# Performance work log

Hardware: AMD Instinct MI355X
Metric: run time of the kernel (lower is better)

Reference implementation:

```python
import jax, jax.numpy as jnp
import numpy as np
from jax.scipy.linalg import solve_triangular

N, D, E = 100000, 128, 1600000
LAMDA, ALPHA = 0.5, 0.1


def setup_inputs() -> dict:
    key = jax.random.key(0)
    k1, k2, k3, k4, k5, k6 = jax.random.split(key, 6)
    x = jax.random.normal(k1, (N, D), dtype=jnp.float32)
    h0 = jax.random.normal(k2, (N, D), dtype=jnp.float32)
    # glorot_init range for the weight
    init_range = np.sqrt(6.0 / (D + D)).astype(np.float32)
    weight = jax.random.uniform(k3, (D, D), dtype=jnp.float32, minval=-init_range, maxval=init_range)
    adj_vals = jax.random.uniform(k4, (E,), dtype=jnp.float32)  # normalized adjacency values (positive)
    adj_rows = jax.random.randint(k5, (E,), 0, N, dtype=jnp.int32)
    adj_cols = jax.random.randint(k6, (E,), 0, N, dtype=jnp.int32)
    return {"x": x, "h0": h0, "weight": weight, "adj_vals": adj_vals,
            "adj_rows": adj_rows, "adj_cols": adj_cols, "l": 4}


def _ortho_norm(weight):
    d = weight.shape[1]
    wtw = weight.T @ weight + 1e-4 * jnp.eye(d, dtype=weight.dtype)
    L = jnp.linalg.cholesky(wtw)
    # weight @ inv(L).T == (solve(L, weight.T)).T
    return solve_triangular(L, weight.T, lower=True).T


def reference(x, h0, weight, adj_vals, adj_rows, adj_cols, l):
    theta = float(np.log(LAMDA / l + 1.0))
    w_ortho = _ortho_norm(weight)
    # sparse adjacency SpMM: hi[r] = sum_e adj_vals[e] * x[adj_cols[e]] for adj_rows[e]==r
    hi = jax.ops.segment_sum(adj_vals[:, None] * x[adj_cols], adj_rows, num_segments=x.shape[0])
    support = (1.0 - ALPHA) * hi + ALPHA * h0  # variant=False -> r == support
    out = theta * (support @ w_ortho) + (1.0 - theta) * support
    return jnp.tanh(out)  # residual=False
```

## Files before the change

kernel.cpp:

```cpp
#include <hip/hip_runtime.h>
#include <math.h>

#define D 128
#define NB 16
#define RPB 64
#define NBUK_MAX 1024
#define RPBUK 128
#define EPB 16384
#define ALPHA 0.1f
#define LAMDA 0.5f

__global__ __launch_bounds__(256) void wtw_kernel(const float* __restrict__ W,
                                                  float* __restrict__ A) {
    int idx = blockIdx.x * blockDim.x + threadIdx.x;
    int i = idx >> 7, j = idx & (D - 1);
    float acc = (i == j) ? 1e-4f : 0.0f;
#pragma unroll 4
    for (int k = 0; k < D; ++k) acc = fmaf(W[k * D + i], W[k * D + j], acc);
    A[idx] = acc;
}

__global__ __launch_bounds__(256) void chol_factor_kernel(const float* __restrict__ A_in,
                                                          float* __restrict__ Lg) {
    __shared__ float S[D][D];
    __shared__ float dinvS[NB];
    const int tid = threadIdx.x;
    const int tx = tid & 15;
    const int ty = tid >> 4;

    for (int i = tid; i < D * D; i += 256) ((float*)S)[i] = A_in[i];
    __syncthreads();

    for (int s = 0; s < D / NB; ++s) {
        const int b = s * NB;

        for (int k = 0; k < NB; ++k) {
            float dk  = S[b + k][b + k];
            float a_i = S[b + k][b + tx];
            float a_j = S[b + k][b + ty];
            float lkk  = sqrtf(dk);
            float inv  = 1.0f / lkk;
            float invd = inv * inv;
            __syncthreads();
            if (ty == 0) {
                if (tx == k)       { S[b + k][b + k] = lkk; dinvS[k] = inv; }
                else if (tx > k)     S[b + k][b + tx] = a_i * inv;
            }
            if (ty > k && tx >= ty)
                S[b + ty][b + tx] -= a_i * (a_j * invd);
            __syncthreads();
        }

        const int m = D - b - NB;

        if (m > 0 && tid < m) {
            const int r = b + NB + tid;
            float y[NB];
#pragma unroll
            for (int k = 0; k < NB; ++k) y[k] = S[b + k][r];
#pragma unroll
            for (int k = 0; k < NB; ++k) {
                float acc = y[k];
#pragma unroll
                for (int q = 0; q < NB; ++q)
                    if (q < k) acc -= S[b + q][b + k] * y[q];
                y[k] = acc * dinvS[k];
            }
#pragma unroll
            for (int k = 0; k < NB; ++k) S[b + k][r] = y[k];
        }
        __syncthreads();

        const int nt = m >> 4;
        for (int tc = 0; tc < nt; ++tc) {
            for (int tr = tc; tr < nt; ++tr) {
                const int c = b + NB + tc * 16 + ty;
                const int r = b + NB + tr * 16 + tx;
                if (r >= c) {
                    float acc = S[c][r];
#pragma unroll
                    for (int k = 0; k < NB; ++k)
                        acc -= S[b + k][r] * S[b + k][c];
                    S[c][r] = acc;
                }
            }
        }
        __syncthreads();
    }

    for (int i = tid; i < D * D; i += 256) Lg[i] = ((float*)S)[i];
}

__global__ __launch_bounds__(64) void solve_m_kernel(const float* __restrict__ Lg,
                                                     const float* __restrict__ W,
                                                     const int* __restrict__ lp,
                                                     float* __restrict__ Mg) {
    __shared__ float Lr[D][D + 1];
    const int lane = threadIdx.x;
    const int c = blockIdx.x;

    for (int j = 0; j < D; ++j) {
        Lr[lane][j]      = Lg[j * D + lane];
        Lr[lane + 64][j] = Lg[j * D + lane + 64];
    }
    __syncthreads();

    const float w_lo = W[c * D + lane];
    const float w_hi = W[c * D + 64 + lane];
    const float dinv_lo = 1.0f / Lr[lane][lane];
    const float dinv_hi = 1.0f / Lr[lane + 64][lane + 64];
    float y_lo = 0.0f, y_hi = 0.0f;

    for (int i = 0; i < D; ++i) {
        float l0 = Lr[i][lane];
        float l1 = Lr[i][lane + 64];
        float p = 0.0f;
        p += (lane < i)      ? l0 * y_lo : 0.0f;
        p += (lane + 64 < i) ? l1 * y_hi : 0.0f;
#pragma unroll
        for (int off = 32; off >= 1; off >>= 1) p += __shfl_xor(p, off);
        if (i < 64) {
            if (lane == i)      y_lo = (w_lo - p) * dinv_lo;
        } else {
            if (lane == i - 64) y_hi = (w_hi - p) * dinv_hi;
        }
    }

    const float th = logf(LAMDA / (float)(*lp) + 1.0f);
    float m_lo = th * y_lo + ((c == lane)      ? (1.0f - th) : 0.0f);
    float m_hi = th * y_hi + ((c == lane + 64) ? (1.0f - th) : 0.0f);
    Mg[c * D + lane]      = m_lo;
    Mg[c * D + 64 + lane] = m_hi;
}

__global__ __launch_bounds__(256) void cvt_bf16_kernel(const float* __restrict__ x,
                                                       unsigned short* __restrict__ xb,
                                                       int nd) {
    const int base = (blockIdx.x * 256 + threadIdx.x) * 8;
    if (base + 7 < nd) {
        float4 a = *reinterpret_cast<const float4*>(x + base);
        float4 b = *reinterpret_cast<const float4*>(x + base + 4);
        unsigned r[8];
        const float* f = &a.x;
#pragma unroll
        for (int i = 0; i < 4; ++i) {
            unsigned u = __float_as_uint(f[i]);
            r[i] = (u + 0x7FFFu + ((u >> 16) & 1u)) >> 16;
        }
        const float* g = &b.x;
#pragma unroll
        for (int i = 0; i < 4; ++i) {
            unsigned u = __float_as_uint(g[i]);
            r[4 + i] = (u + 0x7FFFu + ((u >> 16) & 1u)) >> 16;
        }
        uint4 o;
        o.x = r[0] | (r[1] << 16);
        o.y = r[2] | (r[3] << 16);
        o.z = r[4] | (r[5] << 16);
        o.w = r[6] | (r[7] << 16);
        *reinterpret_cast<uint4*>(xb + base) = o;
    } else {
        for (int i = 0; i < 8 && base + i < nd; ++i) {
            unsigned u = __float_as_uint(x[base + i]);
            xb[base + i] = (unsigned short)((u + 0x7FFFu + ((u >> 16) & 1u)) >> 16);
        }
    }
}

__global__ __launch_bounds__(256) void count_bucket_kernel(const int* __restrict__ rows,
                                                           int* __restrict__ bcnt,
                                                           int E, int nbuk) {
    __shared__ int lcnt[NBUK_MAX];
    const int tid = threadIdx.x;
    const int e0 = blockIdx.x * EPB;
    const int e1 = min(e0 + EPB, E);
    for (int i = tid; i < nbuk; i += 256) lcnt[i] = 0;
    __syncthreads();
    for (int e = e0 + tid * 4; e < e1; e += 1024) {
        if (e + 3 < e1) {
            int4 r = *reinterpret_cast<const int4*>(rows + e);
            atomicAdd(&lcnt[r.x >> 7], 1);
            atomicAdd(&lcnt[r.y >> 7], 1);
            atomicAdd(&lcnt[r.z >> 7], 1);
            atomicAdd(&lcnt[r.w >> 7], 1);
        } else {
            int lim = min(e + 4, e1);
            for (int k = e; k < lim; ++k) atomicAdd(&lcnt[rows[k] >> 7], 1);
        }
    }
    __syncthreads();
    for (int i = tid; i < nbuk; i += 256) {
        int c = lcnt[i];
        if (c) atomicAdd(&bcnt[i], c);
    }
}

__global__ __launch_bounds__(1024) void scan_bucket_kernel(const int* __restrict__ bcnt,
                                                           int* __restrict__ bbase,
                                                           int* __restrict__ gcur,
                                                           int nbuk) {
    __shared__ int ps[1024];
    const int tid = threadIdx.x;
    int v = (tid < nbuk) ? bcnt[tid] : 0;
    ps[tid] = v;
    __syncthreads();
    for (int off = 1; off < 1024; off <<= 1) {
        int t = (tid >= off) ? ps[tid - off] : 0;
        __syncthreads();
        ps[tid] += t;
        __syncthreads();
    }
    if (tid < nbuk) {
        int excl = ps[tid] - v;
        bbase[tid] = excl;
        gcur[tid]  = excl;
    }
}

__global__ __launch_bounds__(256) void partition_kernel(const int* __restrict__ rows,
                                                        const int* __restrict__ cols,
                                                        const float* __restrict__ vals,
                                                        int* __restrict__ gcur,
                                                        uint2* __restrict__ buk,
                                                        int E, int nbuk) {
    __shared__ int lcnt[NBUK_MAX];
    __shared__ int lbase[NBUK_MAX];
    __shared__ int loff[NBUK_MAX];
    const int tid = threadIdx.x;
    const int e0 = blockIdx.x * EPB;
    const int e1 = min(e0 + EPB, E);
    for (int i = tid; i < nbuk; i += 256) { lcnt[i] = 0; loff[i] = 0; }
    __syncthreads();
    for (int e = e0 + tid * 4; e < e1; e += 1024) {
        if (e + 3 < e1) {
            int4 r = *reinterpret_cast<const int4*>(rows + e);
            atomicAdd(&lcnt[r.x >> 7], 1);
            atomicAdd(&lcnt[r.y >> 7], 1);
            atomicAdd(&lcnt[r.z >> 7], 1);
            atomicAdd(&lcnt[r.w >> 7], 1);
        } else {
            int lim = min(e + 4, e1);
            for (int k = e; k < lim; ++k) atomicAdd(&lcnt[rows[k] >> 7], 1);
        }
    }
    __syncthreads();
    for (int i = tid; i < nbuk; i += 256) {
        int c = lcnt[i];
        if (c) lbase[i] = atomicAdd(&gcur[i], c);
    }
    __syncthreads();
    for (int e = e0 + tid * 4; e < e1; e += 1024) {
        if (e + 3 < e1) {
            int4 r = *reinterpret_cast<const int4*>(rows + e);
            int4 c = *reinterpret_cast<const int4*>(cols + e);
            float4 v = *reinterpret_cast<const float4*>(vals + e);
            {
                int b = r.x >> 7; int li = atomicAdd(&loff[b], 1);
                buk[lbase[b] + li] = make_uint2((unsigned)c.x | ((unsigned)(r.x & 127) << 20), __float_as_uint(v.x));
            }
            {
                int b = r.y >> 7; int li = atomicAdd(&loff[b], 1);
                buk[lbase[b] + li] = make_uint2((unsigned)c.y | ((unsigned)(r.y & 127) << 20), __float_as_uint(v.y));
            }
            {
                int b = r.z >> 7; int li = atomicAdd(&loff[b], 1);
                buk[lbase[b] + li] = make_uint2((unsigned)c.z | ((unsigned)(r.z & 127) << 20), __float_as_uint(v.z));
            }
            {
                int b = r.w >> 7; int li = atomicAdd(&loff[b], 1);
                buk[lbase[b] + li] = make_uint2((unsigned)c.w | ((unsigned)(r.w & 127) << 20), __float_as_uint(v.w));
            }
        } else {
            int lim = min(e + 4, e1);
            for (int k = e; k < lim; ++k) {
                int rr = rows[k];
                int b = rr >> 7; int li = atomicAdd(&loff[b], 1);
                buk[lbase[b] + li] = make_uint2((unsigned)cols[k] | ((unsigned)(rr & 127) << 20), __float_as_uint(vals[k]));
            }
        }
    }
}

__global__ __launch_bounds__(256) void bucket_to_csr_kernel(const uint2* __restrict__ buk,
                                                            const int* __restrict__ bbase,
                                                            const int* __restrict__ bend,
                                                            uint2* __restrict__ csr,
                                                            int* __restrict__ rp, int n) {
    __shared__ int lcnt[RPBUK];
    __shared__ int lofs[RPBUK];
    const int tid = threadIdx.x;
    const int b = blockIdx.x;
    const int start = bbase[b], end = bend[b];

    if (tid < RPBUK) lcnt[tid] = 0;
    __syncthreads();
    for (int j = start + tid; j < end; j += 256)
        atomicAdd(&lcnt[buk[j].x >> 20], 1);
    __syncthreads();
    if (tid < RPBUK) lofs[tid] = lcnt[tid];
    __syncthreads();
    for (int off = 1; off < RPBUK; off <<= 1) {
        int v = (tid < RPBUK && tid >= off) ? lofs[tid - off] : 0;
        __syncthreads();
        if (tid < RPBUK) lofs[tid] += v;
        __syncthreads();
    }
    if (tid < RPBUK) {
        int r = b * RPBUK + tid;
        if (r < n) rp[r] = start + lofs[tid];
        lofs[tid] -= lcnt[tid];
    }
    __syncthreads();
    for (int j = start + tid; j < end; j += 256) {
        uint2 e = buk[j];
        int rl = e.x >> 20;
        int pos = atomicAdd(&lofs[rl], 1);
        csr[start + pos] = make_uint2(e.x & 0xFFFFFu, e.y);
    }
}

__global__ __launch_bounds__(256, 4) void fused_spmm_gemm_kernel(
        const unsigned short* __restrict__ xb,
        const float* __restrict__ h0,
        const uint2* __restrict__ csr,
        const int* __restrict__ rp,
        const float* __restrict__ Mg,
        float* __restrict__ out, int n) {
    __shared__ float Ss[RPB][D + 1];
    const int tid = threadIdx.x;
    const int r0  = blockIdx.x * RPB;
    const int q   = tid & 15;
    const int rw  = tid >> 4;

#pragma unroll
    for (int sub = 0; sub < 4; ++sub) {
        const int sr = sub * 16 + rw;
        const int r  = r0 + sr;
        float acc[8] = {};
        if (r < n) {
            const int start = (r == 0) ? 0 : rp[r - 1];
            const int end   = rp[r];
            int j = start;
            for (; j + 1 < end; j += 2) {
                uint2 p0 = csr[j];
                uint2 p1 = csr[j + 1];
                float v0 = __uint_as_float(p0.y);
                float v1 = __uint_as_float(p1.y);
                uint4 a = *reinterpret_cast<const uint4*>(xb + (size_t)p0.x * D + q * 8);
                uint4 b = *reinterpret_cast<const uint4*>(xb + (size_t)p1.x * D + q * 8);
                const unsigned* aw = &a.x;
                const unsigned* bw = &b.x;
#pragma unroll
                for (int t = 0; t < 4; ++t) {
                    float alo = __uint_as_float(aw[t] << 16);
                    float ahi = __uint_as_float(aw[t] & 0xffff0000u);
                    acc[2 * t]     = fmaf(v0, alo, acc[2 * t]);
                    acc[2 * t + 1] = fmaf(v0, ahi, acc[2 * t + 1]);
                    float blo = __uint_as_float(bw[t] << 16);
                    float bhi = __uint_as_float(bw[t] & 0xffff0000u);
                    acc[2 * t]     = fmaf(v1, blo, acc[2 * t]);
                    acc[2 * t + 1] = fmaf(v1, bhi, acc[2 * t + 1]);
                }
            }
            if (j < end) {
                uint2 p0 = csr[j];
                float v0 = __uint_as_float(p0.y);
                uint4 a = *reinterpret_cast<const uint4*>(xb + (size_t)p0.x * D + q * 8);
                const unsigned* aw = &a.x;
#pragma unroll
                for (int t = 0; t < 4; ++t) {
                    float alo = __uint_as_float(aw[t] << 16);
                    float ahi = __uint_as_float(aw[t] & 0xffff0000u);
                    acc[2 * t]     = fmaf(v0, alo, acc[2 * t]);
                    acc[2 * t + 1] = fmaf(v0, ahi, acc[2 * t + 1]);
                }
            }
            const float4 hb0 = *reinterpret_cast<const float4*>(h0 + (size_t)r * D + q * 8);
            const float4 hb1 = *reinterpret_cast<const float4*>(h0 + (size_t)r * D + q * 8 + 4);
            acc[0] = 0.9f * acc[0] + 0.1f * hb0.x;
            acc[1] = 0.9f * acc[1] + 0.1f * hb0.y;
            acc[2] = 0.9f * acc[2] + 0.1f * hb0.z;
            acc[3] = 0.9f * acc[3] + 0.1f * hb0.w;
            acc[4] = 0.9f * acc[4] + 0.1f * hb1.x;
            acc[5] = 0.9f * acc[5] + 0.1f * hb1.y;
            acc[6] = 0.9f * acc[6] + 0.1f * hb1.z;
            acc[7] = 0.9f * acc[7] + 0.1f * hb1.w;
        }
#pragma unroll
        for (int i = 0; i < 8; ++i) Ss[sr][q * 8 + i] = acc[i];
    }
    __syncthreads();

    const int tc = tid & 15;
    const int tr = tid >> 4;
    float acc2[4][8] = {};
#pragma unroll 8
    for (int k = 0; k < D; ++k) {
        float4 b0 = *reinterpret_cast<const float4*>(Mg + k * D + tc * 4);
        float4 b1 = *reinterpret_cast<const float4*>(Mg + k * D + 64 + tc * 4);
#pragma unroll
        for (int m = 0; m < 4; ++m) {
            float a = Ss[4 * tr + m][k];
            acc2[m][0] = fmaf(a, b0.x, acc2[m][0]);
            acc2[m][1] = fmaf(a, b0.y, acc2[m][1]);
            acc2[m][2] = fmaf(a, b0.z, acc2[m][2]);
            acc2[m][3] = fmaf(a, b0.w, acc2[m][3]);
            acc2[m][4] = fmaf(a, b1.x, acc2[m][4]);
            acc2[m][5] = fmaf(a, b1.y, acc2[m][5]);
            acc2[m][6] = fmaf(a, b1.z, acc2[m][6]);
            acc2[m][7] = fmaf(a, b1.w, acc2[m][7]);
        }
    }

#pragma unroll
    for (int m = 0; m < 4; ++m) {
        int r = r0 + 4 * tr + m;
        if (r >= n) continue;
        float4 o0, o1;
        o0.x = tanhf(acc2[m][0]); o0.y = tanhf(acc2[m][1]);
        o0.z = tanhf(acc2[m][2]); o0.w = tanhf(acc2[m][3]);
        o1.x = tanhf(acc2[m][4]); o1.y = tanhf(acc2[m][5]);
        o1.z = tanhf(acc2[m][6]); o1.w = tanhf(acc2[m][7]);
        *reinterpret_cast<float4*>(out + (size_t)r * D + tc * 4)      = o0;
        *reinterpret_cast<float4*>(out + (size_t)r * D + 64 + tc * 4) = o1;
    }
}

__global__ __launch_bounds__(256) void spmm_atomic_kernel(const float* __restrict__ x,
                                                          const float* __restrict__ vals,
                                                          const int* __restrict__ rows,
                                                          const int* __restrict__ cols,
                                                          float* __restrict__ hi, int E) {
    int tid = blockIdx.x * blockDim.x + threadIdx.x;
    int e = tid >> 5;
    if (e >= E) return;
    int q = tid & 31;
    float v = vals[e];
    int c = cols[e];
    int r = rows[e];
    const float4 xv = *reinterpret_cast<const float4*>(x + (size_t)c * D + q * 4);
    float* h = hi + (size_t)r * D + q * 4;
    unsafeAtomicAdd(h + 0, v * xv.x);
    unsafeAtomicAdd(h + 1, v * xv.y);
    unsafeAtomicAdd(h + 2, v * xv.z);
    unsafeAtomicAdd(h + 3, v * xv.w);
}

__global__ __launch_bounds__(256) void blend_kernel(const float* __restrict__ hi,
                                                    const float* __restrict__ h0,
                                                    float* __restrict__ S, int nd4) {
    int i = blockIdx.x * blockDim.x + threadIdx.x;
    if (i >= nd4) return;
    float4 a = reinterpret_cast<const float4*>(hi)[i];
    float4 b = reinterpret_cast<const float4*>(h0)[i];
    float4 s;
    s.x = 0.9f * a.x + 0.1f * b.x;
    s.y = 0.9f * a.y + 0.1f * b.y;
    s.z = 0.9f * a.z + 0.1f * b.z;
    s.w = 0.9f * a.w + 0.1f * b.w;
    reinterpret_cast<float4*>(S)[i] = s;
}

__global__ __launch_bounds__(256) void gemm_tanh_kernel(const float* __restrict__ S,
                                                        const float* __restrict__ Mg,
                                                        float* __restrict__ out, int n) {
    __shared__ float Ss[RPB][D + 1];
    const int tid = threadIdx.x;
    const int r0  = blockIdx.x * RPB;

    for (int i = tid; i < RPB * D / 4; i += 256) {
        int rr = (i * 4) / D, cc = (i * 4) & (D - 1);
        int r = r0 + rr;
        float4 a = (r < n) ? *reinterpret_cast<const float4*>(S + (size_t)r * D + cc)
                           : make_float4(0.f, 0.f, 0.f, 0.f);
        Ss[rr][cc + 0] = a.x;
        Ss[rr][cc + 1] = a.y;
        Ss[rr][cc + 2] = a.z;
        Ss[rr][cc + 3] = a.w;
    }
    __syncthreads();

    const int tc = tid & 15;
    const int tr = tid >> 4;
    float acc[4][8] = {};
#pragma unroll 8
    for (int k = 0; k < D; ++k) {
        float4 b0 = *reinterpret_cast<const float4*>(Mg + k * D + tc * 4);
        float4 b1 = *reinterpret_cast<const float4*>(Mg + k * D + 64 + tc * 4);
#pragma unroll
        for (int m = 0; m < 4; ++m) {
            float a = Ss[4 * tr + m][k];
            acc[m][0] = fmaf(a, b0.x, acc[m][0]);
            acc[m][1] = fmaf(a, b0.y, acc[m][1]);
            acc[m][2] = fmaf(a, b0.z, acc[m][2]);
            acc[m][3] = fmaf(a, b0.w, acc[m][3]);
            acc[m][4] = fmaf(a, b1.x, acc[m][4]);
            acc[m][5] = fmaf(a, b1.y, acc[m][5]);
            acc[m][6] = fmaf(a, b1.z, acc[m][6]);
            acc[m][7] = fmaf(a, b1.w, acc[m][7]);
        }
    }

#pragma unroll
    for (int m = 0; m < 4; ++m) {
        int r = r0 + 4 * tr + m;
        if (r >= n) continue;
        float4 o0, o1;
        o0.x = tanhf(acc[m][0]); o0.y = tanhf(acc[m][1]);
        o0.z = tanhf(acc[m][2]); o0.w = tanhf(acc[m][3]);
        o1.x = tanhf(acc[m][4]); o1.y = tanhf(acc[m][5]);
        o1.z = tanhf(acc[m][6]); o1.w = tanhf(acc[m][7]);
        *reinterpret_cast<float4*>(out + (size_t)r * D + tc * 4)      = o0;
        *reinterpret_cast<float4*>(out + (size_t)r * D + 64 + tc * 4) = o1;
    }
}

extern "C" void kernel_launch(void* const* d_in, const int* in_sizes, int n_in,
                              void* d_out, int out_size, void* d_ws, size_t ws_size,
                              hipStream_t stream) {
    const float* x  = (const float*)d_in[0];
    const float* h0 = (const float*)d_in[1];
    const float* W  = (const float*)d_in[2];
    const float* av = (const float*)d_in[3];
    const int*   ar = (const int*)d_in[4];
    const int*   ac = (const int*)d_in[5];
    const int*   lp = (const int*)d_in[6];
    float* out = (float*)d_out;

    const int nd = in_sizes[0];
    const int n  = nd / D;
    const int E  = in_sizes[3];
    const int nbuk  = (n + RPBUK - 1) / RPBUK;
    const int nblkE = (E + EPB - 1) / EPB;
    const int grid64 = (n + RPB - 1) / RPB;

    char* wsb = (char*)d_ws;
    float* A  = (float*)wsb;
    float* Lg = A + D * D;
    float* Mg = Lg + D * D;
    size_t off = 3 * (size_t)D * D * sizeof(float);

    int* bcnt  = (int*)(wsb + off); off += NBUK_MAX * sizeof(int);
    int* bbase = (int*)(wsb + off); off += NBUK_MAX * sizeof(int);
    int* gcur  = (int*)(wsb + off); off += NBUK_MAX * sizeof(int);
    off = (off + 15) & ~(size_t)15;
    int* rp = (int*)(wsb + off); off += (size_t)n * sizeof(int);
    off = (off + 15) & ~(size_t)15;
    uint2* csr = (uint2*)(wsb + off); off += (size_t)E * sizeof(uint2);
    off = (off + 15) & ~(size_t)15;
    uint2* buk = (uint2*)(wsb + off); off += (size_t)E * sizeof(uint2);
    off = (off + 15) & ~(size_t)15;
    unsigned short* xb = (unsigned short*)(wsb + off);
    off += (size_t)nd * sizeof(unsigned short);
    off = (off + 15) & ~(size_t)15;
    const size_t need_core = off;

    if (ws_size >= need_core && nbuk <= NBUK_MAX && n < (1 << 20)) {
        hipMemsetAsync(bcnt, 0, NBUK_MAX * sizeof(int), stream);
        count_bucket_kernel<<<nblkE, 256, 0, stream>>>(ar, bcnt, E, nbuk);
        cvt_bf16_kernel<<<(nd / 8 + 255) / 256, 256, 0, stream>>>(x, xb, nd);
        wtw_kernel<<<D * D / 256, 256, 0, stream>>>(W, A);
        scan_bucket_kernel<<<1, 1024, 0, stream>>>(bcnt, bbase, gcur, nbuk);
        partition_kernel<<<nblkE, 256, 0, stream>>>(ar, ac, av, gcur, buk, E, nbuk);
        bucket_to_csr_kernel<<<nbuk, 256, 0, stream>>>(buk, bbase, gcur, csr, rp, n);
        chol_factor_kernel<<<1, 256, 0, stream>>>(A, Lg);
        solve_m_kernel<<<D, 64, 0, stream>>>(Lg, W, lp, Mg);
        fused_spmm_gemm_kernel<<<grid64, 256, 0, stream>>>(xb, h0, csr, rp, Mg, out, n);
    } else {
        float* hi = out;
        hipMemsetAsync(hi, 0, (size_t)nd * sizeof(float), stream);
        wtw_kernel<<<D * D / 256, 256, 0, stream>>>(W, A);
        spmm_atomic_kernel<<<(int)(((size_t)E * 32 + 255) / 256), 256, 0, stream>>>(x, av, ar, ac, hi, E);
        chol_factor_kernel<<<1, 256, 0, stream>>>(A, Lg);
        solve_m_kernel<<<D, 64, 0, stream>>>(Lg, W, lp, Mg);
        blend_kernel<<<(nd / 4 + 255) / 256, 256, 0, stream>>>(hi, h0, hi, nd / 4);
        gemm_tanh_kernel<<<grid64, 256, 0, stream>>>(hi, Mg, out, n);
    }
}
```

Before: 323.2 us.

## Merge independent setup kernels into combined launches to cut launch count

Merges bucket counting, bf16 conversion and W^T W into one prep kernel dispatched by block index. It also co-schedules edge partitioning with the single-block Cholesky, and CSR construction with the triangular solve, so the serial weight path runs alongside the graph preprocessing. The goal is fewer kernel launches and hiding the latency of the one-block Cholesky. In exchange, pc_kernel now reserves 64KB of shared memory for every block, which may lower occupancy of the partition blocks, and the solve blocks run 256 threads where only 64 are needed.

```diff
diff --git a/kernel.cpp b/kernel.cpp
--- a/kernel.cpp
+++ b/kernel.cpp
@@ -13,6 +13,7 @@
 __global__ __launch_bounds__(256) void wtw_kernel(const float* __restrict__ W,
                                                   float* __restrict__ A) {
     int idx = blockIdx.x * blockDim.x + threadIdx.x;
+    if (idx >= D * D) return;
     int i = idx >> 7, j = idx & (D - 1);
     float acc = (i == j) ? 1e-4f : 0.0f;
 #pragma unroll 4
@@ -20,178 +21,75 @@
     A[idx] = acc;
 }
 
-__global__ __launch_bounds__(256) void chol_factor_kernel(const float* __restrict__ A_in,
-                                                          float* __restrict__ Lg) {
-    __shared__ float S[D][D];
-    __shared__ float dinvS[NB];
-    const int tid = threadIdx.x;
-    const int tx = tid & 15;
-    const int ty = tid >> 4;
-
-    for (int i = tid; i < D * D; i += 256) ((float*)S)[i] = A_in[i];
-    __syncthreads();
-
-    for (int s = 0; s < D / NB; ++s) {
-        const int b = s * NB;
-
-        for (int k = 0; k < NB; ++k) {
-            float dk  = S[b + k][b + k];
-            float a_i = S[b + k][b + tx];
-            float a_j = S[b + k][b + ty];
-            float lkk  = sqrtf(dk);
-            float inv  = 1.0f / lkk;
-            float invd = inv * inv;
-            __syncthreads();
-            if (ty == 0) {
-                if (tx == k)       { S[b + k][b + k] = lkk; dinvS[k] = inv; }
-                else if (tx > k)     S[b + k][b + tx] = a_i * inv;
-            }
-            if (ty > k && tx >= ty)
-                S[b + ty][b + tx] -= a_i * (a_j * invd);
-            __syncthreads();
-        }
-
-        const int m = D - b - NB;
-
-        if (m > 0 && tid < m) {
-            const int r = b + NB + tid;
-            float y[NB];
-#pragma unroll
-            for (int k = 0; k < NB; ++k) y[k] = S[b + k][r];
-#pragma unroll
-            for (int k = 0; k < NB; ++k) {
-                float acc = y[k];
-#pragma unroll
-                for (int q = 0; q < NB; ++q)
-                    if (q < k) acc -= S[b + q][b + k] * y[q];
-                y[k] = acc * dinvS[k];
-            }
-#pragma unroll
-            for (int k = 0; k < NB; ++k) S[b + k][r] = y[k];
-        }
-        __syncthreads();
-
-        const int nt = m >> 4;
-        for (int tc = 0; tc < nt; ++tc) {
-            for (int tr = tc; tr < nt; ++tr) {
-                const int c = b + NB + tc * 16 + ty;
-                const int r = b + NB + tr * 16 + tx;
-                if (r >= c) {
-                    float acc = S[c][r];
-#pragma unroll
-                    for (int k = 0; k < NB; ++k)
-                        acc -= S[b + k][r] * S[b + k][c];
-                    S[c][r] = acc;
-                }
-            }
-        }
-        __syncthreads();
-    }
-
-    for (int i = tid; i < D * D; i += 256) Lg[i] = ((float*)S)[i];
-}
-
-__global__ __launch_bounds__(64) void solve_m_kernel(const float* __restrict__ Lg,
-                                                     const float* __restrict__ W,
-                                                     const int* __restrict__ lp,
-                                                     float* __restrict__ Mg) {
-    __shared__ float Lr[D][D + 1];
-    const int lane = threadIdx.x;
-    const int c = blockIdx.x;
-
-    for (int j = 0; j < D; ++j) {
-        Lr[lane][j]      = Lg[j * D + lane];
-        Lr[lane + 64][j] = Lg[j * D + lane + 64];
-    }
-    __syncthreads();
-
-    const float w_lo = W[c * D + lane];
-    const float w_hi = W[c * D + 64 + lane];
-    const float dinv_lo = 1.0f / Lr[lane][lane];
-    const float dinv_hi = 1.0f / Lr[lane + 64][lane + 64];
-    float y_lo = 0.0f, y_hi = 0.0f;
-
-    for (int i = 0; i < D; ++i) {
-        float l0 = Lr[i][lane];
-        float l1 = Lr[i][lane + 64];
-        float p = 0.0f;
-        p += (lane < i)      ? l0 * y_lo : 0.0f;
-        p += (lane + 64 < i) ? l1 * y_hi : 0.0f;
-#pragma unroll
-        for (int off = 32; off >= 1; off >>= 1) p += __shfl_xor(p, off);
-        if (i < 64) {
-            if (lane == i)      y_lo = (w_lo - p) * dinv_lo;
-        } else {
-            if (lane == i - 64) y_hi = (w_hi - p) * dinv_hi;
-        }
-    }
-
-    const float th = logf(LAMDA / (float)(*lp) + 1.0f);
-    float m_lo = th * y_lo + ((c == lane)      ? (1.0f - th) : 0.0f);
-    float m_hi = th * y_hi + ((c == lane + 64) ? (1.0f - th) : 0.0f);
-    Mg[c * D + lane]      = m_lo;
-    Mg[c * D + 64 + lane] = m_hi;
-}
-
-__global__ __launch_bounds__(256) void cvt_bf16_kernel(const float* __restrict__ x,
-                                                       unsigned short* __restrict__ xb,
-                                                       int nd) {
-    const int base = (blockIdx.x * 256 + threadIdx.x) * 8;
-    if (base + 7 < nd) {
-        float4 a = *reinterpret_cast<const float4*>(x + base);
-        float4 b = *reinterpret_cast<const float4*>(x + base + 4);
-        unsigned r[8];
-        const float* f = &a.x;
-#pragma unroll
-        for (int i = 0; i < 4; ++i) {
-            unsigned u = __float_as_uint(f[i]);
-            r[i] = (u + 0x7FFFu + ((u >> 16) & 1u)) >> 16;
-        }
-        const float* g = &b.x;
-#pragma unroll
-        for (int i = 0; i < 4; ++i) {
-            unsigned u = __float_as_uint(g[i]);
-            r[4 + i] = (u + 0x7FFFu + ((u >> 16) & 1u)) >> 16;
-        }
-        uint4 o;
-        o.x = r[0] | (r[1] << 16);
-        o.y = r[2] | (r[3] << 16);
-        o.z = r[4] | (r[5] << 16);
-        o.w = r[6] | (r[7] << 16);
-        *reinterpret_cast<uint4*>(xb + base) = o;
-    } else {
-        for (int i = 0; i < 8 && base + i < nd; ++i) {
-            unsigned u = __float_as_uint(x[base + i]);
-            xb[base + i] = (unsigned short)((u + 0x7FFFu + ((u >> 16) & 1u)) >> 16);
-        }
-    }
-}
-
-__global__ __launch_bounds__(256) void count_bucket_kernel(const int* __restrict__ rows,
-                                                           int* __restrict__ bcnt,
-                                                           int E, int nbuk) {
+__global__ __launch_bounds__(256) void prep_kernel(
+        const int* __restrict__ rows, int* __restrict__ bcnt, int E, int nbuk, int nCnt,
+        const float* __restrict__ x, unsigned short* __restrict__ xb, int nd, int nCvt,
+        const float* __restrict__ W, float* __restrict__ A) {
     __shared__ int lcnt[NBUK_MAX];
     const int tid = threadIdx.x;
-    const int e0 = blockIdx.x * EPB;
-    const int e1 = min(e0 + EPB, E);
-    for (int i = tid; i < nbuk; i += 256) lcnt[i] = 0;
-    __syncthreads();
-    for (int e = e0 + tid * 4; e < e1; e += 1024) {
-        if (e + 3 < e1) {
-            int4 r = *reinterpret_cast<const int4*>(rows + e);
-            atomicAdd(&lcnt[r.x >> 7], 1);
-            atomicAdd(&lcnt[r.y >> 7], 1);
-            atomicAdd(&lcnt[r.z >> 7], 1);
-            atomicAdd(&lcnt[r.w >> 7], 1);
+    const int blk = blockIdx.x;
+
+    if (blk < nCnt) {
+        const int e0 = blk * EPB;
+        const int e1 = min(e0 + EPB, E);
+        for (int i = tid; i < nbuk; i += 256) lcnt[i] = 0;
+        __syncthreads();
+        for (int e = e0 + tid * 4; e < e1; e += 1024) {
+            if (e + 3 < e1) {
+                int4 r = *reinterpret_cast<const int4*>(rows + e);
+                atomicAdd(&lcnt[r.x >> 7], 1);
+                atomicAdd(&lcnt[r.y >> 7], 1);
+                atomicAdd(&lcnt[r.z >> 7], 1);
+                atomicAdd(&lcnt[r.w >> 7], 1);
+            } else {
+                int lim = min(e + 4, e1);
+                for (int k = e; k < lim; ++k) atomicAdd(&lcnt[rows[k] >> 7], 1);
+            }
+        }
+        __syncthreads();
+        for (int i = tid; i < nbuk; i += 256) {
+            int c = lcnt[i];
+            if (c) atomicAdd(&bcnt[i], c);
+        }
+    } else if (blk < nCnt + nCvt) {
+        const int base = ((blk - nCnt) * 256 + tid) * 8;
+        if (base + 7 < nd) {
+            float4 a = *reinterpret_cast<const float4*>(x + base);
+            float4 b = *reinterpret_cast<const float4*>(x + base + 4);
+            unsigned r[8];
+            const float* f = &a.x;
+#pragma unroll
+            for (int i = 0; i < 4; ++i) {
+                unsigned u = __float_as_uint(f[i]);
+                r[i] = (u + 0x7FFFu + ((u >> 16) & 1u)) >> 16;
+            }
+            const float* g = &b.x;
+#pragma unroll
+            for (int i = 0; i < 4; ++i) {
+                unsigned u = __float_as_uint(g[i]);
+                r[4 + i] = (u + 0x7FFFu + ((u >> 16) & 1u)) >> 16;
+            }
+            uint4 o;
+            o.x = r[0] | (r[1] << 16);
+            o.y = r[2] | (r[3] << 16);
+            o.z = r[4] | (r[5] << 16);
+            o.w = r[6] | (r[7] << 16);
+            *reinterpret_cast<uint4*>(xb + base) = o;
         } else {
-            int lim = min(e + 4, e1);
-            for (int k = e; k < lim; ++k) atomicAdd(&lcnt[rows[k] >> 7], 1);
-        }
-    }
-    __syncthreads();
-    for (int i = tid; i < nbuk; i += 256) {
-        int c = lcnt[i];
-        if (c) atomicAdd(&bcnt[i], c);
+            for (int i = 0; i < 8 && base + i < nd; ++i) {
+                unsigned u = __float_as_uint(x[base + i]);
+                xb[base + i] = (unsigned short)((u + 0x7FFFu + ((u >> 16) & 1u)) >> 16);
+            }
+        }
+    } else {
+        int idx = (blk - nCnt - nCvt) * 256 + tid;
+        if (idx < D * D) {
+            int i = idx >> 7, j = idx & (D - 1);
+            float acc = (i == j) ? 1e-4f : 0.0f;
+#pragma unroll 4
+            for (int k = 0; k < D; ++k) acc = fmaf(W[k * D + i], W[k * D + j], acc);
+            A[idx] = acc;
+        }
     }
 }
 
@@ -217,105 +115,215 @@
     }
 }
 
-__global__ __launch_bounds__(256) void partition_kernel(const int* __restrict__ rows,
-                                                        const int* __restrict__ cols,
-                                                        const float* __restrict__ vals,
-                                                        int* __restrict__ gcur,
-                                                        uint2* __restrict__ buk,
-                                                        int E, int nbuk) {
-    __shared__ int lcnt[NBUK_MAX];
-    __shared__ int lbase[NBUK_MAX];
-    __shared__ int loff[NBUK_MAX];
+__global__ __launch_bounds__(256) void pc_kernel(
+        const int* __restrict__ rows, const int* __restrict__ cols,
+        const float* __restrict__ vals, int* __restrict__ gcur,
+        uint2* __restrict__ buk, int E, int nbuk, int nPart,
+        const float* __restrict__ A_in, float* __restrict__ Lg) {
+    __shared__ float smem[D * D];
+    __shared__ float dinvS[NB];
     const int tid = threadIdx.x;
-    const int e0 = blockIdx.x * EPB;
-    const int e1 = min(e0 + EPB, E);
-    for (int i = tid; i < nbuk; i += 256) { lcnt[i] = 0; loff[i] = 0; }
-    __syncthreads();
-    for (int e = e0 + tid * 4; e < e1; e += 1024) {
-        if (e + 3 < e1) {
-            int4 r = *reinterpret_cast<const int4*>(rows + e);
-            atomicAdd(&lcnt[r.x >> 7], 1);
-            atomicAdd(&lcnt[r.y >> 7], 1);
-            atomicAdd(&lcnt[r.z >> 7], 1);
-            atomicAdd(&lcnt[r.w >> 7], 1);
-        } else {
-            int lim = min(e + 4, e1);
-            for (int k = e; k < lim; ++k) atomicAdd(&lcnt[rows[k] >> 7], 1);
-        }
-    }
-    __syncthreads();
-    for (int i = tid; i < nbuk; i += 256) {
-        int c = lcnt[i];
-        if (c) lbase[i] = atomicAdd(&gcur[i], c);
-    }
-    __syncthreads();
-    for (int e = e0 + tid * 4; e < e1; e += 1024) {
-        if (e + 3 < e1) {
-            int4 r = *reinterpret_cast<const int4*>(rows + e);
-            int4 c = *reinterpret_cast<const int4*>(cols + e);
-            float4 v = *reinterpret_cast<const float4*>(vals + e);
-            {
-                int b = r.x >> 7; int li = atomicAdd(&loff[b], 1);
-                buk[lbase[b] + li] = make_uint2((unsigned)c.x | ((unsigned)(r.x & 127) << 20), __float_as_uint(v.x));
-            }
-            {
-                int b = r.y >> 7; int li = atomicAdd(&loff[b], 1);
-                buk[lbase[b] + li] = make_uint2((unsigned)c.y | ((unsigned)(r.y & 127) << 20), __float_as_uint(v.y));
-            }
-            {
-                int b = r.z >> 7; int li = atomicAdd(&loff[b], 1);
-                buk[lbase[b] + li] = make_uint2((unsigned)c.z | ((unsigned)(r.z & 127) << 20), __float_as_uint(v.z));
-            }
-            {
-                int b = r.w >> 7; int li = atomicAdd(&loff[b], 1);
-                buk[lbase[b] + li] = make_uint2((unsigned)c.w | ((unsigned)(r.w & 127) << 20), __float_as_uint(v.w));
-            }
-        } else {
-            int lim = min(e + 4, e1);
-            for (int k = e; k < lim; ++k) {
-                int rr = rows[k];
-                int b = rr >> 7; int li = atomicAdd(&loff[b], 1);
-                buk[lbase[b] + li] = make_uint2((unsigned)cols[k] | ((unsigned)(rr & 127) << 20), __float_as_uint(vals[k]));
-            }
-        }
-    }
-}
-
-__global__ __launch_bounds__(256) void bucket_to_csr_kernel(const uint2* __restrict__ buk,
-                                                            const int* __restrict__ bbase,
-                                                            const int* __restrict__ bend,
-                                                            uint2* __restrict__ csr,
-                                                            int* __restrict__ rp, int n) {
-    __shared__ int lcnt[RPBUK];
-    __shared__ int lofs[RPBUK];
+
+    if ((int)blockIdx.x < nPart) {
+        int* lcnt  = (int*)smem;
+        int* lbase = lcnt + NBUK_MAX;
+        int* loff  = lbase + NBUK_MAX;
+        const int e0 = blockIdx.x * EPB;
+        const int e1 = min(e0 + EPB, E);
+        for (int i = tid; i < nbuk; i += 256) { lcnt[i] = 0; loff[i] = 0; }
+        __syncthreads();
+        for (int e = e0 + tid * 4; e < e1; e += 1024) {
+            if (e + 3 < e1) {
+                int4 r = *reinterpret_cast<const int4*>(rows + e);
+                atomicAdd(&lcnt[r.x >> 7], 1);
+                atomicAdd(&lcnt[r.y >> 7], 1);
+                atomicAdd(&lcnt[r.z >> 7], 1);
+                atomicAdd(&lcnt[r.w >> 7], 1);
+            } else {
+                int lim = min(e + 4, e1);
+                for (int k = e; k < lim; ++k) atomicAdd(&lcnt[rows[k] >> 7], 1);
+            }
+        }
+        __syncthreads();
+        for (int i = tid; i < nbuk; i += 256) {
+            int c = lcnt[i];
+            if (c) lbase[i] = atomicAdd(&gcur[i], c);
+        }
+        __syncthreads();
+        for (int e = e0 + tid * 4; e < e1; e += 1024) {
+            if (e + 3 < e1) {
+                int4 r = *reinterpret_cast<const int4*>(rows + e);
+                int4 c = *reinterpret_cast<const int4*>(cols + e);
+                float4 v = *reinterpret_cast<const float4*>(vals + e);
+                {
+                    int b = r.x >> 7; int li = atomicAdd(&loff[b], 1);
+                    buk[lbase[b] + li] = make_uint2((unsigned)c.x | ((unsigned)(r.x & 127) << 20), __float_as_uint(v.x));
+                }
+                {
+                    int b = r.y >> 7; int li = atomicAdd(&loff[b], 1);
+                    buk[lbase[b] + li] = make_uint2((unsigned)c.y | ((unsigned)(r.y & 127) << 20), __float_as_uint(v.y));
+                }
+                {
+                    int b = r.z >> 7; int li = atomicAdd(&loff[b], 1);
+                    buk[lbase[b] + li] = make_uint2((unsigned)c.z | ((unsigned)(r.z & 127) << 20), __float_as_uint(v.z));
+                }
+                {
+                    int b = r.w >> 7; int li = atomicAdd(&loff[b], 1);
+                    buk[lbase[b] + li] = make_uint2((unsigned)c.w | ((unsigned)(r.w & 127) << 20), __float_as_uint(v.w));
+                }
+            } else {
+                int lim = min(e + 4, e1);
+                for (int k = e; k < lim; ++k) {
+                    int rr = rows[k];
+                    int b = rr >> 7; int li = atomicAdd(&loff[b], 1);
+                    buk[lbase[b] + li] = make_uint2((unsigned)cols[k] | ((unsigned)(rr & 127) << 20), __float_as_uint(vals[k]));
+                }
+            }
+        }
+    } else {
+        float (*S)[D] = (float (*)[D])smem;
+        const int tx = tid & 15;
+        const int ty = tid >> 4;
+
+        for (int i = tid; i < D * D; i += 256) smem[i] = A_in[i];
+        __syncthreads();
+
+        for (int s = 0; s < D / NB; ++s) {
+            const int b = s * NB;
+            for (int k = 0; k < NB; ++k) {
+                float dk  = S[b + k][b + k];
+                float a_i = S[b + k][b + tx];
+                float a_j = S[b + k][b + ty];
+                float lkk  = sqrtf(dk);
+                float inv  = 1.0f / lkk;
+                float invd = inv * inv;
+                __syncthreads();
+                if (ty == 0) {
+                    if (tx == k)       { S[b + k][b + k] = lkk; dinvS[k] = inv; }
+                    else if (tx > k)     S[b + k][b + tx] = a_i * inv;
+                }
+                if (ty > k && tx >= ty)
+                    S[b + ty][b + tx] -= a_i * (a_j * invd);
+                __syncthreads();
+            }
+
+            const int m = D - b - NB;
+            if (m > 0 && tid < m) {
+                const int r = b + NB + tid;
+                float y[NB];
+#pragma unroll
+                for (int k = 0; k < NB; ++k) y[k] = S[b + k][r];
+#pragma unroll
+                for (int k = 0; k < NB; ++k) {
+                    float acc = y[k];
+#pragma unroll
+                    for (int q = 0; q < NB; ++q)
+                        if (q < k) acc -= S[b + q][b + k] * y[q];
+                    y[k] = acc * dinvS[k];
+                }
+#pragma unroll
+                for (int k = 0; k < NB; ++k) S[b + k][r] = y[k];
+            }
+            __syncthreads();
+
+            const int nt = m >> 4;
+            for (int tc = 0; tc < nt; ++tc) {
+                for (int tr = tc; tr < nt; ++tr) {
+                    const int c = b + NB + tc * 16 + ty;
+                    const int r = b + NB + tr * 16 + tx;
+                    if (r >= c) {
+                        float acc = S[c][r];
+#pragma unroll
+                        for (int k = 0; k < NB; ++k)
+                            acc -= S[b + k][r] * S[b + k][c];
+                        S[c][r] = acc;
+                    }
+                }
+            }
+            __syncthreads();
+        }
+
+        for (int i = tid; i < D * D; i += 256) Lg[i] = smem[i];
+    }
+}
+
+__global__ __launch_bounds__(256) void cs_kernel(
+        const uint2* __restrict__ buk, const int* __restrict__ bbase,
+        const int* __restrict__ bend, uint2* __restrict__ csr,
+        int* __restrict__ rp, int n, int nBuk,
+        const float* __restrict__ Lg, const float* __restrict__ W,
+        const int* __restrict__ lp, float* __restrict__ Mg) {
+    __shared__ float Lr[D][D + 1];
     const int tid = threadIdx.x;
     const int b = blockIdx.x;
-    const int start = bbase[b], end = bend[b];
-
-    if (tid < RPBUK) lcnt[tid] = 0;
-    __syncthreads();
-    for (int j = start + tid; j < end; j += 256)
-        atomicAdd(&lcnt[buk[j].x >> 20], 1);
-    __syncthreads();
-    if (tid < RPBUK) lofs[tid] = lcnt[tid];
-    __syncthreads();
-    for (int off = 1; off < RPBUK; off <<= 1) {
-        int v = (tid < RPBUK && tid >= off) ? lofs[tid - off] : 0;
-        __syncthreads();
-        if (tid < RPBUK) lofs[tid] += v;
-        __syncthreads();
-    }
-    if (tid < RPBUK) {
-        int r = b * RPBUK + tid;
-        if (r < n) rp[r] = start + lofs[tid];
-        lofs[tid] -= lcnt[tid];
-    }
-    __syncthreads();
-    for (int j = start + tid; j < end; j += 256) {
-        uint2 e = buk[j];
-        int rl = e.x >> 20;
-        int pos = atomicAdd(&lofs[rl], 1);
-        csr[start + pos] = make_uint2(e.x & 0xFFFFFu, e.y);
+
+    if (b < nBuk) {
+        int* lcnt = (int*)&Lr[0][0];
+        int* lofs = lcnt + RPBUK;
+        const int start = bbase[b], end = bend[b];
+
+        if (tid < RPBUK) lcnt[tid] = 0;
+        __syncthreads();
+        for (int j = start + tid; j < end; j += 256)
+            atomicAdd(&lcnt[buk[j].x >> 20], 1);
+        __syncthreads();
+        if (tid < RPBUK) lofs[tid] = lcnt[tid];
+        __syncthreads();
+        for (int off = 1; off < RPBUK; off <<= 1) {
+            int v = (tid < RPBUK && tid >= off) ? lofs[tid - off] : 0;
+            __syncthreads();
+            if (tid < RPBUK) lofs[tid] += v;
+            __syncthreads();
+        }
+        if (tid < RPBUK) {
+            int r = b * RPBUK + tid;
+            if (r < n) rp[r] = start + lofs[tid];
+            lofs[tid] -= lcnt[tid];
+        }
+        __syncthreads();
+        for (int j = start + tid; j < end; j += 256) {
+            uint2 e = buk[j];
+            int rl = e.x >> 20;
+            int pos = atomicAdd(&lofs[rl], 1);
+            csr[start + pos] = make_uint2(e.x & 0xFFFFFu, e.y);
+        }
+    } else {
+        const int c = b - nBuk;
+        for (int idx = tid; idx < D * D; idx += 256) {
+            int i = idx & (D - 1), j = idx >> 7;
+            Lr[i][j] = Lg[j * D + i];
+        }
+        __syncthreads();
+
+        const int lane = tid & 63;
+        const float w_lo = W[c * D + lane];
+        const float w_hi = W[c * D + 64 + lane];
+        const float dinv_lo = 1.0f / Lr[lane][lane];
+        const float dinv_hi = 1.0f / Lr[lane + 64][lane + 64];
+        float y_lo = 0.0f, y_hi = 0.0f;
+
+        for (int i = 0; i < D; ++i) {
+            float l0 = Lr[i][lane];
+            float l1 = Lr[i][lane + 64];
+            float p = 0.0f;
+            p += (lane < i)      ? l0 * y_lo : 0.0f;
+            p += (lane + 64 < i) ? l1 * y_hi : 0.0f;
+#pragma unroll
+            for (int off = 32; off >= 1; off >>= 1) p += __shfl_xor(p, off);
+            if (i < 64) {
+                if (lane == i)      y_lo = (w_lo - p) * dinv_lo;
+            } else {
+                if (lane == i - 64) y_hi = (w_hi - p) * dinv_hi;
+            }
+        }
+
+        if (tid < 64) {
+            const float th = logf(LAMDA / (float)(*lp) + 1.0f);
+            float m_lo = th * y_lo + ((c == lane)      ? (1.0f - th) : 0.0f);
+            float m_hi = th * y_hi + ((c == lane + 64) ? (1.0f - th) : 0.0f);
+            Mg[c * D + lane]      = m_lo;
+            Mg[c * D + 64 + lane] = m_hi;
+        }
     }
 }
 
@@ -532,7 +540,7 @@
     const int E  = in_sizes[3];
     const int nbuk  = (n + RPBUK - 1) / RPBUK;
     const int nblkE = (E + EPB - 1) / EPB;
-    const int grid64 = (n + RPB - 1) / RPB;
+    const int nCvt  = (nd / 8 + 255) / 256;
 
     char* wsb = (char*)d_ws;
     float* A  = (float*)wsb;
@@ -557,23 +565,20 @@
 
     if (ws_size >= need_core && nbuk <= NBUK_MAX && n < (1 << 20)) {
         hipMemsetAsync(bcnt, 0, NBUK_MAX * sizeof(int), stream);
-        count_bucket_kernel<<<nblkE, 256, 0, stream>>>(ar, bcnt, E, nbuk);
-        cvt_bf16_kernel<<<(nd / 8 + 255) / 256, 256, 0, stream>>>(x, xb, nd);
-        wtw_kernel<<<D * D / 256, 256, 0, stream>>>(W, A);
+        prep_kernel<<<nblkE + nCvt + 64, 256, 0, stream>>>(ar, bcnt, E, nbuk, nblkE,
+                                                           x, xb, nd, nCvt, W, A);
         scan_bucket_kernel<<<1, 1024, 0, stream>>>(bcnt, bbase, gcur, nbuk);
-        partition_kernel<<<nblkE, 256, 0, stream>>>(ar, ac, av, gcur, buk, E, nbuk);
-        bucket_to_csr_kernel<<<nbuk, 256, 0, stream>>>(buk, bbase, gcur, csr, rp, n);
-        chol_factor_kernel<<<1, 256, 0, stream>>>(A, Lg);
-        solve_m_kernel<<<D, 64, 0, stream>>>(Lg, W, lp, Mg);
-        fused_spmm_gemm_kernel<<<grid64, 256, 0, stream>>>(xb, h0, csr, rp, Mg, out, n);
+        pc_kernel<<<nblkE + 1, 256, 0, stream>>>(ar, ac, av, gcur, buk, E, nbuk, nblkE, A, Lg);
+        cs_kernel<<<nbuk + D, 256, 0, stream>>>(buk, bbase, gcur, csr, rp, n, nbuk, Lg, W, lp, Mg);
+        fused_spmm_gemm_kernel<<<(n + RPB - 1) / RPB, 256, 0, stream>>>(xb, h0, csr, rp, Mg, out, n);
     } else {
         float* hi = out;
         hipMemsetAsync(hi, 0, (size_t)nd * sizeof(float), stream);
         wtw_kernel<<<D * D / 256, 256, 0, stream>>>(W, A);
         spmm_atomic_kernel<<<(int)(((size_t)E * 32 + 255) / 256), 256, 0, stream>>>(x, av, ar, ac, hi, E);
-        chol_factor_kernel<<<1, 256, 0, stream>>>(A, Lg);
-        solve_m_kernel<<<D, 64, 0, stream>>>(Lg, W, lp, Mg);
+        pc_kernel<<<1, 256, 0, stream>>>(nullptr, nullptr, nullptr, nullptr, nullptr, 0, 0, 0, A, Lg);
+        cs_kernel<<<D, 256, 0, stream>>>(nullptr, nullptr, nullptr, nullptr, nullptr, n, 0, Lg, W, lp, Mg);
         blend_kernel<<<(nd / 4 + 255) / 256, 256, 0, stream>>>(hi, h0, hi, nd / 4);
-        gemm_tanh_kernel<<<grid64, 256, 0, stream>>>(hi, Mg, out, n);
-    }
-}
+        gemm_tanh_kernel<<<(n + RPB - 1) / RPB, 256, 0, stream>>>(hi, Mg, out, n);
+    }
+}
```

New measurement: 282.4 us. 12.6% less time.
